# Performance work log

Measured on AMD Instinct MI355X. Metric: run time of the kernel, lower is better.

The kernel has to match this reference:

```python
import jax, jax.numpy as jnp
import numpy as np

DIM = 1024
HEADS = 16
DIM_HEAD = 64
INNER = HEADS * DIM_HEAD
EPS = 1e-6


def elu_feature_map(t):
    # F.elu(x) + 1
    return jnp.where(t > 0, t + 1.0, jnp.exp(t))


def setup_inputs() -> dict:
    key = jax.random.key(0)
    k1, k2, k3, k4 = jax.random.split(key, 4)
    B, N = 4, 8192
    x = jax.random.normal(k1, (B, N, DIM), dtype=jnp.float32)
    s_in = 1.0 / np.sqrt(DIM)
    s_out = 1.0 / np.sqrt(INNER)
    Wqkv = jax.random.uniform(k2, (DIM, 3 * INNER), dtype=jnp.float32, minval=-s_in, maxval=s_in)
    Wout = jax.random.uniform(k3, (INNER, DIM), dtype=jnp.float32, minval=-s_out, maxval=s_out)
    bout = jax.random.uniform(k4, (DIM,), dtype=jnp.float32, minval=-s_out, maxval=s_out)
    return {"x": x, "Wqkv": Wqkv, "Wout": Wout, "bout": bout}


def reference(x, Wqkv, Wout, bout):
    B, N, D = x.shape
    qkv = x @ Wqkv  # [B,N,3*INNER]
    q, k, v = jnp.split(qkv, 3, axis=-1)
    # b n (h d) -> b h n d
    resh = lambda t: t.reshape(B, N, HEADS, DIM_HEAD).transpose(0, 2, 1, 3)
    q, k, v = resh(q), resh(k), resh(v)
    q = elu_feature_map(q)
    k = elu_feature_map(k)
    kv = jnp.einsum('bhnd,bhnf->bhdf', k, v)          # [B,H,d,d]
    k_sum = k.sum(axis=-2)                             # [B,H,d]
    qkv_out = jnp.einsum('bhnd,bhdf->bhnf', q, kv)    # [B,H,N,d]
    q_k_sum = jnp.einsum('bhnd,bhd->bhn', q, k_sum)   # [B,H,N]
    out = qkv_out / (q_k_sum[..., None] + EPS)
    out = out.transpose(0, 2, 1, 3).reshape(B, N, INNER)  # b h n d -> b n (h d)
    return out @ Wout + bout
```

## Files before the change

### kernel.cpp

```cpp
#include <hip/hip_runtime.h>
#include <hip/hip_bf16.h>
#include <math.h>


typedef unsigned short ushort_t;
typedef __attribute__((ext_vector_type(8))) short s8v;
typedef __attribute__((ext_vector_type(4))) float f32x4;

#define MFMA(a,b,c) __builtin_amdgcn_mfma_f32_16x16x32_bf16((a),(b),(c),0,0,0)

typedef __attribute__((address_space(3))) unsigned int as3_u32;
typedef __attribute__((address_space(1))) const unsigned int as1_u32c;

__device__ __forceinline__ void g2l16(const void* g, void* l) {
    __builtin_amdgcn_global_load_lds((as1_u32c*)g, (as3_u32*)l, 16, 0, 0);
}

__device__ __forceinline__ float bf2f(ushort_t u) {
    union { float f; unsigned v; } x; x.v = ((unsigned)u) << 16; return x.f;
}
__device__ __forceinline__ ushort_t f2bf(float f) {
    union { float f; unsigned v; } x; x.f = f;
    unsigned r = x.v + 0x7fffu + ((x.v >> 16) & 1u);
    return (ushort_t)(r >> 16);
}
__device__ __forceinline__ float elu1(float t) { return t > 0.0f ? t + 1.0f : expf(t); }

__global__ void k_cast(const float* __restrict__ in, ushort_t* __restrict__ out, int n8) {
    int i = blockIdx.x * blockDim.x + threadIdx.x;
    if (i >= n8) return;
    const float4* p = (const float4*)in;
    float4 a = p[(size_t)i * 2], b = p[(size_t)i * 2 + 1];
    uint4 o;
    o.x = (unsigned)f2bf(a.x) | ((unsigned)f2bf(a.y) << 16);
    o.y = (unsigned)f2bf(a.z) | ((unsigned)f2bf(a.w) << 16);
    o.z = (unsigned)f2bf(b.x) | ((unsigned)f2bf(b.y) << 16);
    o.w = (unsigned)f2bf(b.z) | ((unsigned)f2bf(b.w) << 16);
    *(uint4*)(out + (size_t)i * 8) = o;
}

__global__ __launch_bounds__(256) void k_transpose(const float* __restrict__ W,
                                                   ushort_t* __restrict__ WT, int K, int N) {
    __shared__ float s[32][33];
    const int t = threadIdx.x;
    const int k0 = blockIdx.x * 32, n0 = blockIdx.y * 32;
    const int kr = t >> 3, n4 = (t & 7) * 4;
    float4 v = *(const float4*)(W + (size_t)(k0 + kr) * N + n0 + n4);
    s[kr][n4 + 0] = v.x; s[kr][n4 + 1] = v.y; s[kr][n4 + 2] = v.z; s[kr][n4 + 3] = v.w;
    __syncthreads();
    const int nr = kr, k4 = n4;
    unsigned lo = (unsigned)f2bf(s[k4 + 0][nr]) | ((unsigned)f2bf(s[k4 + 1][nr]) << 16);
    unsigned hi = (unsigned)f2bf(s[k4 + 2][nr]) | ((unsigned)f2bf(s[k4 + 3][nr]) << 16);
    *(uint2*)(WT + (size_t)(n0 + nr) * K + k0 + k4) = make_uint2(lo, hi);
}

template<int MODE>
__global__ __launch_bounds__(512, 2) void k_gemm(
    const ushort_t* __restrict__ A, const ushort_t* __restrict__ B,
    ushort_t* __restrict__ obf, const float* __restrict__ bout, float* __restrict__ of)
{
    constexpr int ASZ  = 256 * 64;
    constexpr int BUFS = 2 * ASZ;
    __shared__ ushort_t lds[2 * BUFS];

    const int t = threadIdx.x, l = t & 63, w = t >> 6;
    const int wr = w >> 2, wc = w & 3;
    const size_t m0 = (size_t)blockIdx.x * 256;
    const size_t n0 = (size_t)blockIdx.y * 256;

    f32x4 acc[8][4];
    const f32x4 z = {0.f, 0.f, 0.f, 0.f};
#pragma unroll
    for (int i = 0; i < 8; i++)
#pragma unroll
        for (int j = 0; j < 4; j++) acc[i][j] = z;

    const int lr  = l >> 3;
    const int lco = ((l & 7) ^ lr) << 3;
    const ushort_t* gA = A + (m0 + (size_t)(32 * w) + lr) * 1024 + lco;
    const ushort_t* gB = B + (n0 + (size_t)(32 * w) + lr) * 1024 + lco;
    const int la15 = l & 15;
    const int exo  = (((l >> 4) ^ (l & 7)) << 3);

#pragma unroll
    for (int i = 0; i < 4; i++)
        g2l16(gA + (size_t)(8 * i) * 1024, &lds[(w * 4 + i) * 512]);
#pragma unroll
    for (int i = 0; i < 4; i++)
        g2l16(gB + (size_t)(8 * i) * 1024, &lds[ASZ + (w * 4 + i) * 512]);
    asm volatile("s_waitcnt vmcnt(0)" ::: "memory");
    __builtin_amdgcn_sched_barrier(0);
    __builtin_amdgcn_s_barrier();
    __builtin_amdgcn_sched_barrier(0);

    for (int T = 0; T < 16; ++T) {
        const int base  = (T & 1) * BUFS;
        const int nbase = BUFS - base;

        if (T < 15) {
            const size_t k1 = (size_t)(T + 1) * 64;
#pragma unroll
            for (int i = 0; i < 4; i++)
                g2l16(gA + (size_t)(8 * i) * 1024 + k1, &lds[nbase + (w * 4 + i) * 512]);
#pragma unroll
            for (int i = 0; i < 4; i++)
                g2l16(gB + (size_t)(8 * i) * 1024 + k1, &lds[nbase + ASZ + (w * 4 + i) * 512]);
        }

        s8v af[8], bf[4];
#pragma unroll
        for (int nf = 0; nf < 4; nf++)
            bf[nf] = *(const s8v*)&lds[base + ASZ + (wc * 64 + nf * 16 + la15) * 64 + exo];
#pragma unroll
        for (int mf = 0; mf < 8; mf++)
            af[mf] = *(const s8v*)&lds[base + (wr * 128 + mf * 16 + la15) * 64 + exo];
        __builtin_amdgcn_s_setprio(1);
#pragma unroll
        for (int mf = 0; mf < 8; mf++)
#pragma unroll
            for (int nf = 0; nf < 4; nf++)
                acc[mf][nf] = MFMA(af[mf], bf[nf], acc[mf][nf]);
        __builtin_amdgcn_s_setprio(0);
#pragma unroll
        for (int nf = 0; nf < 4; nf++)
            bf[nf] = *(const s8v*)&lds[base + ASZ + (wc * 64 + nf * 16 + la15) * 64 + (32 ^ exo)];
#pragma unroll
        for (int mf = 0; mf < 8; mf++)
            af[mf] = *(const s8v*)&lds[base + (wr * 128 + mf * 16 + la15) * 64 + (32 ^ exo)];
        __builtin_amdgcn_s_setprio(1);
#pragma unroll
        for (int mf = 0; mf < 8; mf++)
#pragma unroll
            for (int nf = 0; nf < 4; nf++)
                acc[mf][nf] = MFMA(af[mf], bf[nf], acc[mf][nf]);
        __builtin_amdgcn_s_setprio(0);

        if (T < 15) {
            __builtin_amdgcn_sched_barrier(0);
            asm volatile("s_waitcnt vmcnt(0)" ::: "memory");
            __builtin_amdgcn_sched_barrier(0);
            __builtin_amdgcn_s_barrier();
            __builtin_amdgcn_sched_barrier(0);
        }
    }

    const int r4 = (l >> 4) * 4;
    if (MODE == 0) {
#pragma unroll
        for (int mf = 0; mf < 8; mf++)
#pragma unroll
            for (int nf = 0; nf < 4; nf++) {
                const size_t colb = n0 + wc * 64 + nf * 16;
                const bool feat = colb < 2048;
#pragma unroll
                for (int r = 0; r < 4; r++) {
                    const size_t row = m0 + wr * 128 + mf * 16 + r4 + r;
                    float v = acc[mf][nf][r];
                    obf[row * 3072 + colb + la15] = f2bf(feat ? elu1(v) : v);
                }
            }
    } else {
#pragma unroll
        for (int mf = 0; mf < 8; mf++)
#pragma unroll
            for (int nf = 0; nf < 4; nf++) {
                const size_t col = n0 + wc * 64 + nf * 16 + la15;
                const float bo = bout[col];
#pragma unroll
                for (int r = 0; r < 4; r++) {
                    const size_t row = m0 + wr * 128 + mf * 16 + r4 + r;
                    of[row * 1024 + col] = acc[mf][nf][r] + bo;
                }
            }
    }
}

#define KST 136
__global__ __launch_bounds__(256) void k_kv(
    const ushort_t* __restrict__ qkv, float* __restrict__ kv, float* __restrict__ ksum)
{
    __shared__ ushort_t kT[64 * KST];
    __shared__ ushort_t vT[64 * KST];
    __shared__ float ksl[64];
    const int t = threadIdx.x, l = t & 63, w = t >> 6;
    const int wr = w >> 1, wc = w & 1;
    const int h = blockIdx.x;
    const int b = blockIdx.z;
    const ushort_t* qkvb = qkv + (size_t)b * 8192 * 3072;
    float* kvh = kv + ((size_t)b * 16 + h) * 4096;
    float* ksh = ksum + (size_t)b * 1024 + h * 64;
    const int n00 = blockIdx.y * 512;
    const f32x4 z = {0.f, 0.f, 0.f, 0.f};
    f32x4 acc[2][2] = {{z, z}, {z, z}};
    float ksloc[4] = {0.f, 0.f, 0.f, 0.f};
    const int sd0 = (t & 15) * 4;
    if (t < 64) ksl[t] = 0.f;

    for (int c = 0; c < 4; c++) {
        __syncthreads();
        const int n0 = n00 + c * 128;
#pragma unroll
        for (int i = 0; i < 8; i++) {
            int n = i * 16 + (t >> 4);
            const ushort_t* kp = qkvb + (size_t)(n0 + n) * 3072 + 1024 + h * 64 + sd0;
            ushort4 kw = *(const ushort4*)kp;
            ushort4 vw = *(const ushort4*)(kp + 1024);
            ksloc[0] += bf2f(kw.x); ksloc[1] += bf2f(kw.y);
            ksloc[2] += bf2f(kw.z); ksloc[3] += bf2f(kw.w);
            kT[(sd0 + 0) * KST + n] = kw.x; kT[(sd0 + 1) * KST + n] = kw.y;
            kT[(sd0 + 2) * KST + n] = kw.z; kT[(sd0 + 3) * KST + n] = kw.w;
            vT[(sd0 + 0) * KST + n] = vw.x; vT[(sd0 + 1) * KST + n] = vw.y;
            vT[(sd0 + 2) * KST + n] = vw.z; vT[(sd0 + 3) * KST + n] = vw.w;
        }
        __syncthreads();
#pragma unroll
        for (int kb = 0; kb < 128; kb += 32) {
            s8v af[2], bfr[2];
#pragma unroll
            for (int ma = 0; ma < 2; ma++) {
                int d = wr * 32 + ma * 16 + (l & 15);
                af[ma] = *(const s8v*)&kT[d * KST + kb + (l >> 4) * 8];
            }
#pragma unroll
            for (int fb = 0; fb < 2; fb++) {
                int f = wc * 32 + fb * 16 + (l & 15);
                bfr[fb] = *(const s8v*)&vT[f * KST + kb + (l >> 4) * 8];
            }
#pragma unroll
            for (int ma = 0; ma < 2; ma++)
#pragma unroll
                for (int fb = 0; fb < 2; fb++)
                    acc[ma][fb] = MFMA(af[ma], bfr[fb], acc[ma][fb]);
        }
    }
    atomicAdd(&ksl[sd0 + 0], ksloc[0]); atomicAdd(&ksl[sd0 + 1], ksloc[1]);
    atomicAdd(&ksl[sd0 + 2], ksloc[2]); atomicAdd(&ksl[sd0 + 3], ksloc[3]);
    __syncthreads();
    if (t < 64) atomicAdd(&ksh[t], ksl[t]);
#pragma unroll
    for (int ma = 0; ma < 2; ma++)
#pragma unroll
        for (int fb = 0; fb < 2; fb++)
#pragma unroll
            for (int r = 0; r < 4; r++) {
                int d = wr * 32 + ma * 16 + (l >> 4) * 4 + r;
                int f = wc * 32 + fb * 16 + (l & 15);
                atomicAdd(&kvh[f * 64 + d], acc[ma][fb][r]);
            }
}

#define AST 72
__global__ __launch_bounds__(256) void k_apply(
    const ushort_t* __restrict__ qkv, const float* __restrict__ kv,
    const float* __restrict__ ksum, ushort_t* __restrict__ attn)
{
    __shared__ ushort_t kvb[64 * AST];
    const int t = threadIdx.x, l = t & 63, w = t >> 6;
    const int la15 = l & 15;
    const int row0 = blockIdx.x * 32;
    const int b = row0 >> 13;
    const f32x4 z = {0.f, 0.f, 0.f, 0.f};

    for (int hh = 0; hh < 8; hh++) {
        const int h = blockIdx.y * 8 + hh;
        const float* kvh = kv + ((size_t)b * 16 + h) * 4096;
        const float* ksh = ksum + (size_t)b * 1024 + h * 64;
        __syncthreads();
        {
            const int f = t >> 2, d0 = (t & 3) * 16;
            const float* src = kvh + f * 64 + d0;
            s8v v0, v1;
#pragma unroll
            for (int j = 0; j < 8; j++) {
                v0[j] = (short)f2bf(src[j]);
                v1[j] = (short)f2bf(src[j + 8]);
            }
            *(s8v*)&kvb[f * AST + d0]     = v0;
            *(s8v*)&kvb[f * AST + d0 + 8] = v1;
        }
        __syncthreads();
        float ksv[16];
        {
            const float* kp = ksh + (l >> 4) * 8;
            *(float4*)&ksv[0]  = *(const float4*)(kp);
            *(float4*)&ksv[4]  = *(const float4*)(kp + 4);
            *(float4*)&ksv[8]  = *(const float4*)(kp + 32);
            *(float4*)&ksv[12] = *(const float4*)(kp + 36);
        }
        f32x4 acc[2] = {z, z};
        float pd[2] = {0.f, 0.f};
#pragma unroll
        for (int ks = 0; ks < 2; ks++) {
            const int f = w * 16 + la15;
            s8v bfr = *(const s8v*)&kvb[f * AST + ks * 32 + (l >> 4) * 8];
#pragma unroll
            for (int ma = 0; ma < 2; ma++) {
                int row = row0 + ma * 16 + la15;
                s8v afr = *(const s8v*)(qkv + (size_t)row * 3072 + h * 64 + ks * 32 + (l >> 4) * 8);
#pragma unroll
                for (int j = 0; j < 8; j++)
                    pd[ma] += bf2f((ushort_t)afr[j]) * ksv[ks * 8 + j];
                acc[ma] = MFMA(afr, bfr, acc[ma]);
            }
        }
#pragma unroll
        for (int ma = 0; ma < 2; ma++) {
            pd[ma] += __shfl_xor(pd[ma], 16, 64);
            pd[ma] += __shfl_xor(pd[ma], 32, 64);
        }
#pragma unroll
        for (int ma = 0; ma < 2; ma++)
#pragma unroll
            for (int r = 0; r < 4; r++) {
                int lrow = (l >> 4) * 4 + r;
                float dot = __shfl(pd[ma], lrow, 64);
                float dv = 1.f / (dot + 1e-6f);
                int row = row0 + ma * 16 + lrow;
                int f = w * 16 + la15;
                attn[(size_t)row * 1024 + h * 64 + f] = f2bf(acc[ma][r] * dv);
            }
    }
}

extern "C" void kernel_launch(void* const* d_in, const int* in_sizes, int n_in,
                              void* d_out, int out_size, void* d_ws, size_t ws_size,
                              hipStream_t stream) {
    const float* x    = (const float*)d_in[0];
    const float* Wqkv = (const float*)d_in[1];
    const float* Wout = (const float*)d_in[2];
    const float* bout = (const float*)d_in[3];
    float* out = (float*)d_out;
    char* ws = (char*)d_ws;

    ushort_t* WqkvT = (ushort_t*)(ws + 0);
    ushort_t* WoutT = (ushort_t*)(ws + 6291456);
    float*    kv    = (float*)(ws + 8388608);
    float*    ksum  = (float*)(ws + 12582912);
    ushort_t* xb    = (ushort_t*)(ws + 12599296);
    ushort_t* qkv   = (ushort_t*)(ws + 79708160);
    ushort_t* attn  = (ushort_t*)(ws + 281034752);

    k_transpose<<<dim3(32, 96), 256, 0, stream>>>(Wqkv, WqkvT, 1024, 3072);
    k_transpose<<<dim3(32, 32), 256, 0, stream>>>(Wout, WoutT, 1024, 1024);
    hipMemsetAsync(kv, 0, 4194304 + 16384, stream);
    k_cast<<<16384, 256, 0, stream>>>(x, xb, 4194304);

    k_gemm<0><<<dim3(128, 12), 512, 0, stream>>>(xb, WqkvT, qkv, nullptr, nullptr);
    k_kv<<<dim3(16, 16, 4), 256, 0, stream>>>(qkv, kv, ksum);
    k_apply<<<dim3(1024, 2), 256, 0, stream>>>(qkv, kv, ksum, attn);
    k_gemm<1><<<dim3(128, 4), 512, 0, stream>>>(attn, WoutT, nullptr, bout, out);
}
```

Before: 518.3 us.

## Split GEMM K-tile into half-planes with partial vmcnt waits for finer overlap

The GEMM's LDS staging now splits each 64-wide K tile into two 32-wide planes for A and B, with a new swizzle. Loads for the next tile's first half are issued after the barrier, and loads for the second half are issued mid-iteration. The waits use vmcnt(4) instead of vmcnt(0), so global-to-LDS transfers overlap MFMA work at half-tile granularity rather than draining fully once per tile. Launch bounds drop the minimum blocks per CU from 2 to 1, which gives more register freedom but may lower occupancy. It also adds a second barrier per iteration.

```diff
diff --git a/kernel.cpp b/kernel.cpp
--- a/kernel.cpp
+++ b/kernel.cpp
@@ -55,12 +55,12 @@
 }
 
 template<int MODE>
-__global__ __launch_bounds__(512, 2) void k_gemm(
+__global__ __launch_bounds__(512, 1) void k_gemm(
     const ushort_t* __restrict__ A, const ushort_t* __restrict__ B,
     ushort_t* __restrict__ obf, const float* __restrict__ bout, float* __restrict__ of)
 {
-    constexpr int ASZ  = 256 * 64;
-    constexpr int BUFS = 2 * ASZ;
+    constexpr int PLANE = 256 * 32;
+    constexpr int BUFS  = 4 * PLANE;
     __shared__ ushort_t lds[2 * BUFS];
 
     const int t = threadIdx.x, l = t & 63, w = t >> 6;
@@ -75,45 +75,45 @@
 #pragma unroll
         for (int j = 0; j < 4; j++) acc[i][j] = z;
 
-    const int lr  = l >> 3;
-    const int lco = ((l & 7) ^ lr) << 3;
-    const ushort_t* gA = A + (m0 + (size_t)(32 * w) + lr) * 1024 + lco;
-    const ushort_t* gB = B + (n0 + (size_t)(32 * w) + lr) * 1024 + lco;
+    const int swz = (((l & 3) ^ ((l >> 3) & 3)) << 3);
+    const ushort_t* gAl = A + (m0 + (size_t)(w * 16) + (l >> 2)) * 1024 + swz;
+    const ushort_t* gBl = B + (n0 + (size_t)(w * 16) + (l >> 2)) * 1024 + swz;
+    const int dRow = (w * 16) * 32;
+
     const int la15 = l & 15;
-    const int exo  = (((l >> 4) ^ (l & 7)) << 3);
-
-#pragma unroll
-    for (int i = 0; i < 4; i++)
-        g2l16(gA + (size_t)(8 * i) * 1024, &lds[(w * 4 + i) * 512]);
-#pragma unroll
-    for (int i = 0; i < 4; i++)
-        g2l16(gB + (size_t)(8 * i) * 1024, &lds[ASZ + (w * 4 + i) * 512]);
-    asm volatile("s_waitcnt vmcnt(0)" ::: "memory");
-    __builtin_amdgcn_sched_barrier(0);
-    __builtin_amdgcn_s_barrier();
-    __builtin_amdgcn_sched_barrier(0);
+    const int sA = (((l >> 4) ^ ((la15 >> 1) & 3)) << 3);
+
+    g2l16(gAl,               &lds[0 * PLANE + dRow]);
+    g2l16(gAl + 128 * 1024,  &lds[0 * PLANE + 128 * 32 + dRow]);
+    g2l16(gBl,               &lds[1 * PLANE + dRow]);
+    g2l16(gBl + 128 * 1024,  &lds[1 * PLANE + 128 * 32 + dRow]);
+    g2l16(gAl + 32,              &lds[2 * PLANE + dRow]);
+    g2l16(gAl + 128 * 1024 + 32, &lds[2 * PLANE + 128 * 32 + dRow]);
+    g2l16(gBl + 32,              &lds[3 * PLANE + dRow]);
+    g2l16(gBl + 128 * 1024 + 32, &lds[3 * PLANE + 128 * 32 + dRow]);
 
     for (int T = 0; T < 16; ++T) {
         const int base  = (T & 1) * BUFS;
         const int nbase = BUFS - base;
-
+        const size_t kT1 = (size_t)(T + 1) * 64;
+        s8v af[8], bf[4];
+
+        asm volatile("s_waitcnt vmcnt(4)" ::: "memory");
+        __builtin_amdgcn_sched_barrier(0);
+        __builtin_amdgcn_s_barrier();
+        __builtin_amdgcn_sched_barrier(0);
         if (T < 15) {
-            const size_t k1 = (size_t)(T + 1) * 64;
-#pragma unroll
-            for (int i = 0; i < 4; i++)
-                g2l16(gA + (size_t)(8 * i) * 1024 + k1, &lds[nbase + (w * 4 + i) * 512]);
-#pragma unroll
-            for (int i = 0; i < 4; i++)
-                g2l16(gB + (size_t)(8 * i) * 1024 + k1, &lds[nbase + ASZ + (w * 4 + i) * 512]);
-        }
-
-        s8v af[8], bf[4];
+            g2l16(gAl + kT1,              &lds[nbase + 0 * PLANE + dRow]);
+            g2l16(gAl + 128 * 1024 + kT1, &lds[nbase + 0 * PLANE + 128 * 32 + dRow]);
+            g2l16(gBl + kT1,              &lds[nbase + 1 * PLANE + dRow]);
+            g2l16(gBl + 128 * 1024 + kT1, &lds[nbase + 1 * PLANE + 128 * 32 + dRow]);
+        }
 #pragma unroll
         for (int nf = 0; nf < 4; nf++)
-            bf[nf] = *(const s8v*)&lds[base + ASZ + (wc * 64 + nf * 16 + la15) * 64 + exo];
-#pragma unroll
-        for (int mf = 0; mf < 8; mf++)
-            af[mf] = *(const s8v*)&lds[base + (wr * 128 + mf * 16 + la15) * 64 + exo];
+            bf[nf] = *(const s8v*)&lds[base + 1 * PLANE + (wc * 64 + nf * 16 + la15) * 32 + sA];
+#pragma unroll
+        for (int mf = 0; mf < 8; mf++)
+            af[mf] = *(const s8v*)&lds[base + 0 * PLANE + (wr * 128 + mf * 16 + la15) * 32 + sA];
         __builtin_amdgcn_s_setprio(1);
 #pragma unroll
         for (int mf = 0; mf < 8; mf++)
@@ -121,12 +121,24 @@
             for (int nf = 0; nf < 4; nf++)
                 acc[mf][nf] = MFMA(af[mf], bf[nf], acc[mf][nf]);
         __builtin_amdgcn_s_setprio(0);
+
+        if (T < 15) asm volatile("s_waitcnt vmcnt(4)" ::: "memory");
+        else        asm volatile("s_waitcnt vmcnt(0)" ::: "memory");
+        __builtin_amdgcn_sched_barrier(0);
+        __builtin_amdgcn_s_barrier();
+        __builtin_amdgcn_sched_barrier(0);
+        if (T < 15) {
+            g2l16(gAl + 32 + kT1,              &lds[nbase + 2 * PLANE + dRow]);
+            g2l16(gAl + 128 * 1024 + 32 + kT1, &lds[nbase + 2 * PLANE + 128 * 32 + dRow]);
+            g2l16(gBl + 32 + kT1,              &lds[nbase + 3 * PLANE + dRow]);
+            g2l16(gBl + 128 * 1024 + 32 + kT1, &lds[nbase + 3 * PLANE + 128 * 32 + dRow]);
+        }
 #pragma unroll
         for (int nf = 0; nf < 4; nf++)
-            bf[nf] = *(const s8v*)&lds[base + ASZ + (wc * 64 + nf * 16 + la15) * 64 + (32 ^ exo)];
-#pragma unroll
-        for (int mf = 0; mf < 8; mf++)
-            af[mf] = *(const s8v*)&lds[base + (wr * 128 + mf * 16 + la15) * 64 + (32 ^ exo)];
+            bf[nf] = *(const s8v*)&lds[base + 3 * PLANE + (wc * 64 + nf * 16 + la15) * 32 + sA];
+#pragma unroll
+        for (int mf = 0; mf < 8; mf++)
+            af[mf] = *(const s8v*)&lds[base + 2 * PLANE + (wr * 128 + mf * 16 + la15) * 32 + sA];
         __builtin_amdgcn_s_setprio(1);
 #pragma unroll
         for (int mf = 0; mf < 8; mf++)
@@ -134,14 +146,6 @@
             for (int nf = 0; nf < 4; nf++)
                 acc[mf][nf] = MFMA(af[mf], bf[nf], acc[mf][nf]);
         __builtin_amdgcn_s_setprio(0);
-
-        if (T < 15) {
-            __builtin_amdgcn_sched_barrier(0);
-            asm volatile("s_waitcnt vmcnt(0)" ::: "memory");
-            __builtin_amdgcn_sched_barrier(0);
-            __builtin_amdgcn_s_barrier();
-            __builtin_amdgcn_sched_barrier(0);
-        }
     }
 
     const int r4 = (l >> 4) * 4;
```

Result: slower. 540.5 us (+4.3%).
